# Optimization experiments

Hardware: AMD Instinct MI355X
Metric: run time of the kernel (lower is better)

Reference implementation:

```python
import jax, jax.numpy as jnp
import numpy as np

BN_EPS = 1e-5


def spmm(rows, cols, vals, x):
    # Sparse [V,V] @ x for x: [B, V, F]. COO (rows, cols, vals) with E nnz.
    B, V, F = x.shape
    xt = jnp.transpose(x, (1, 0, 2)).reshape(V, B * F)      # [V, B*F]
    msg = xt[cols] * vals[:, None]                           # [E, B*F]
    y = jax.ops.segment_sum(msg, rows, num_segments=V)       # [V, B*F]
    return jnp.transpose(y.reshape(V, B, F), (1, 0, 2))      # [B, V, F]


def cheb_conv(rows, cols, vals, x, W, b):
    # Chebyshev graph conv: out = sum_k T_k(L) x @ W[k] + b ; W: [K, Fin, Fout]
    K = W.shape[0]
    x0 = x
    out = jnp.einsum('bvi,io->bvo', x0, W[0])
    if K > 1:
        x1 = spmm(rows, cols, vals, x0)
        out = out + jnp.einsum('bvi,io->bvo', x1, W[1])
        for k in range(2, K):
            x2 = 2.0 * spmm(rows, cols, vals, x1) - x0
            out = out + jnp.einsum('bvi,io->bvo', x2, W[k])
            x0, x1 = x1, x2
    return out + b


def bn_relu(x, gamma, beta):
    # BatchNorm1d (training stats) over (batch, nodes) per channel, then ReLU.
    m = jnp.mean(x, axis=(0, 1))
    v = jnp.var(x, axis=(0, 1))
    y = (x - m) * jax.lax.rsqrt(v + BN_EPS) * gamma + beta
    return jax.nn.relu(y)


def setup_inputs() -> dict:
    key = jax.random.key(0)
    ks = jax.random.split(key, 8)
    V, DEG, B, CIN, COUT = 49152, 20, 2, 128, 64
    x = jax.random.normal(ks[0], (B, V, CIN), dtype=jnp.float32)
    # HEALPix-like sparse Laplacian: diagonal + 20 random neighbors per node
    self_idx = jnp.arange(V, dtype=jnp.int32)
    nbr = jax.random.randint(ks[1], (V * DEG,), 0, V, dtype=jnp.int32)
    rows = jnp.concatenate([self_idx, jnp.repeat(self_idx, DEG)])
    cols = jnp.concatenate([self_idx, nbr])
    vals = jax.random.normal(ks[2], (V * (DEG + 1),), dtype=jnp.float32) * 0.1
    def w(k, shape):
        fan_in = shape[0] * shape[1]
        return jax.random.normal(k, shape, dtype=jnp.float32) * np.float32(np.sqrt(2.0 / fan_in))
    return {
        'x': x, 'rows': rows, 'cols': cols, 'vals': vals,
        'W1': w(ks[3], (1, CIN, COUT)), 'b1': jnp.zeros((COUT,), jnp.float32),
        'g1': jnp.ones((COUT,), jnp.float32), 'be1': jnp.zeros((COUT,), jnp.float32),
        'W2': w(ks[4], (3, COUT, COUT)), 'b2': jnp.zeros((COUT,), jnp.float32),
        'g2': jnp.ones((COUT,), jnp.float32), 'be2': jnp.zeros((COUT,), jnp.float32),
        'W3': w(ks[5], (1, COUT, CIN)), 'b3': jnp.zeros((CIN,), jnp.float32),
        'g3': jnp.ones((CIN,), jnp.float32), 'be3': jnp.zeros((CIN,), jnp.float32),
    }


def reference(x, rows, cols, vals, W1, b1, g1, be1, W2, b2, g2, be2, W3, b3, g3, be3):
    h = bn_relu(cheb_conv(rows, cols, vals, x, W1, b1), g1, be1)   # [B,V,64]
    h = bn_relu(cheb_conv(rows, cols, vals, h, W2, b2), g2, be2)   # [B,V,64]
    h = bn_relu(cheb_conv(rows, cols, vals, h, W3, b3), g3, be3)   # [B,V,128]
    return h
```

## Files before the change

### kernel.cpp

```cpp
#include <hip/hip_runtime.h>

#define VN 49152
#define DEG 20
#define NB 2
#define MROWS (NB * VN)

static constexpr float BN_EPS = 1e-5f;

typedef short bf16x8 __attribute__((ext_vector_type(8)));
typedef float floatx4 __attribute__((ext_vector_type(4)));

__device__ __forceinline__ unsigned short f2bf(float f) {
  unsigned int u = __builtin_bit_cast(unsigned int, f);
  u += 0x7FFFu + ((u >> 16) & 1u);
  return (unsigned short)(u >> 16);
}
__device__ __forceinline__ float bf2f(unsigned short h) {
  unsigned int u = ((unsigned int)h) << 16;
  return __builtin_bit_cast(float, u);
}
__device__ __forceinline__ float bflo(unsigned int u) {
  return __builtin_bit_cast(float, u << 16);
}
__device__ __forceinline__ float bfhi(unsigned int u) {
  return __builtin_bit_cast(float, u & 0xFFFF0000u);
}
__device__ __forceinline__ unsigned int packbf(float a, float b) {
  return (unsigned int)f2bf(a) | ((unsigned int)f2bf(b) << 16);
}


#define LDA1 136
__global__ __launch_bounds__(256) void gemm1(const float* __restrict__ X,
    const float* __restrict__ W, const float* __restrict__ bias,
    unsigned short* __restrict__ Y, float* __restrict__ part) {
  __shared__ unsigned short As[128 * LDA1];
  __shared__ unsigned short Bs[64 * LDA1];
  __shared__ float sred[128];
  int t = threadIdx.x;
  int row0 = blockIdx.x * 128;
  if (t < 128) sred[t] = 0.f;
  const float* Xt = X + (size_t)row0 * 128;
  #pragma unroll
  for (int c = 0; c < 16; ++c) {
    int f4i = c * 256 + t;
    int row = f4i >> 5, k = (f4i & 31) * 4;
    float4 v = *(const float4*)(Xt + row * 128 + k);
    unsigned int p0 = packbf(v.x, v.y);
    unsigned int p1 = packbf(v.z, v.w);
    *(uint2*)(&As[row * LDA1 + k]) = make_uint2(p0, p1);
  }
  #pragma unroll
  for (int c = 0; c < 32; ++c) {
    int f = c * 256 + t;
    int k = f >> 6, n = f & 63;
    Bs[n * LDA1 + k] = f2bf(W[f]);
  }
  __syncthreads();
  int l = t & 63, wv = t >> 6;
  int lr = l & 15, q = l >> 4;
  int m0 = wv * 32;
  floatx4 acc[2][4];
  #pragma unroll
  for (int mi = 0; mi < 2; ++mi)
    #pragma unroll
    for (int ni = 0; ni < 4; ++ni) acc[mi][ni] = (floatx4)(0.f);
  #pragma unroll
  for (int ks = 0; ks < 128; ks += 32) {
    bf16x8 af[2], bfr[4];
    #pragma unroll
    for (int mi = 0; mi < 2; ++mi)
      af[mi] = *(const bf16x8*)(&As[(m0 + mi * 16 + lr) * LDA1 + ks + q * 8]);
    #pragma unroll
    for (int ni = 0; ni < 4; ++ni)
      bfr[ni] = *(const bf16x8*)(&Bs[(ni * 16 + lr) * LDA1 + ks + q * 8]);
    #pragma unroll
    for (int mi = 0; mi < 2; ++mi)
      #pragma unroll
      for (int ni = 0; ni < 4; ++ni)
        acc[mi][ni] = __builtin_amdgcn_mfma_f32_16x16x32_bf16(af[mi], bfr[ni], acc[mi][ni], 0, 0, 0);
  }
  int b = (row0 >= VN) ? 1 : 0;
  int vbase = row0 - b * VN + m0;
  #pragma unroll
  for (int ni = 0; ni < 4; ++ni) {
    int col = ni * 16 + lr;
    float bv = bias[col];
    size_t sub = (size_t)(b * 2 + (col >> 5)) * VN;
    float s = 0.f, s2 = 0.f;
    #pragma unroll
    for (int mi = 0; mi < 2; ++mi)
      #pragma unroll
      for (int r = 0; r < 4; ++r) {
        float y = acc[mi][ni][r] + bv;
        s += y; s2 += y * y;
        int v = vbase + mi * 16 + q * 4 + r;
        Y[(sub + v) * 32 + (col & 31)] = f2bf(y);
      }
    atomicAdd(&sred[col], s);
    atomicAdd(&sred[64 + col], s2);
  }
  __syncthreads();
  if (t < 128) part[(size_t)blockIdx.x * 128 + t] = sred[t];
}

#define LDA2 72
__global__ __launch_bounds__(256) void gemm2(const unsigned short* __restrict__ X0,
    const unsigned short* __restrict__ X1, const unsigned short* __restrict__ X2,
    const float* __restrict__ W, const float* __restrict__ bias,
    unsigned short* __restrict__ Y, float* __restrict__ part) {
  __shared__ unsigned short As[128 * LDA2];
  __shared__ unsigned short Bs[64 * LDA2];
  __shared__ float sred[128];
  int t = threadIdx.x;
  int row0 = blockIdx.x * 128;
  int b = (row0 >= VN) ? 1 : 0;
  int b2 = b * 2;
  int vb0 = row0 - b * VN;
  if (t < 128) sred[t] = 0.f;
  int l = t & 63, wv = t >> 6;
  int lr = l & 15, q = l >> 4;
  int m0 = wv * 32;
  floatx4 acc[2][4];
  #pragma unroll
  for (int mi = 0; mi < 2; ++mi)
    #pragma unroll
    for (int ni = 0; ni < 4; ++ni) acc[mi][ni] = (floatx4)(0.f);

  for (int term = 0; term < 3; ++term) {
    const unsigned short* Xp = (term == 0) ? X0 : (term == 1) ? X1 : X2;
    const float* Wt = W + term * 64 * 64;
    #pragma unroll
    for (int c8 = 0; c8 < 8; ++c8) {
      int i = c8 * 256 + t;
      int row = i >> 4, k = (i & 15) * 4;
      const unsigned short* src = Xp + ((size_t)(b2 + (k >> 5)) * VN + vb0 + row) * 32 + (k & 31);
      *(uint2*)(&As[row * LDA2 + k]) = *(const uint2*)src;
    }
    #pragma unroll
    for (int c = 0; c < 16; ++c) {
      int f = c * 256 + t;
      int k = f >> 6, n = f & 63;
      Bs[n * LDA2 + k] = f2bf(Wt[f]);
    }
    __syncthreads();
    #pragma unroll
    for (int ks = 0; ks < 64; ks += 32) {
      bf16x8 af[2], bfr[4];
      #pragma unroll
      for (int mi = 0; mi < 2; ++mi)
        af[mi] = *(const bf16x8*)(&As[(m0 + mi * 16 + lr) * LDA2 + ks + q * 8]);
      #pragma unroll
      for (int ni = 0; ni < 4; ++ni)
        bfr[ni] = *(const bf16x8*)(&Bs[(ni * 16 + lr) * LDA2 + ks + q * 8]);
      #pragma unroll
      for (int mi = 0; mi < 2; ++mi)
        #pragma unroll
        for (int ni = 0; ni < 4; ++ni)
          acc[mi][ni] = __builtin_amdgcn_mfma_f32_16x16x32_bf16(af[mi], bfr[ni], acc[mi][ni], 0, 0, 0);
    }
    __syncthreads();
  }
  int vbase = vb0 + m0;
  #pragma unroll
  for (int ni = 0; ni < 4; ++ni) {
    int col = ni * 16 + lr;
    float bv = bias[col];
    size_t sub = (size_t)(b2 + (col >> 5)) * VN;
    float s = 0.f, s2 = 0.f;
    #pragma unroll
    for (int mi = 0; mi < 2; ++mi)
      #pragma unroll
      for (int r = 0; r < 4; ++r) {
        float y = acc[mi][ni][r] + bv;
        s += y; s2 += y * y;
        int v = vbase + mi * 16 + q * 4 + r;
        Y[(sub + v) * 32 + (col & 31)] = f2bf(y);
      }
    atomicAdd(&sred[col], s);
    atomicAdd(&sred[64 + col], s2);
  }
  __syncthreads();
  if (t < 128) part[(size_t)blockIdx.x * 128 + t] = sred[t];
}

__global__ __launch_bounds__(256) void gemm3(const unsigned short* __restrict__ X,
    const float* __restrict__ W, const float* __restrict__ bias,
    const float* __restrict__ scsh, unsigned short* __restrict__ Y,
    float* __restrict__ part) {
  __shared__ unsigned short As[128 * LDA2];
  __shared__ unsigned short Bs[64 * LDA2];
  __shared__ float sred[128];
  int t = threadIdx.x;
  int row0 = blockIdx.x * 128;
  int n0 = blockIdx.y * 64;
  int b = (row0 >= VN) ? 1 : 0;
  int b2 = b * 2;
  int vb0 = row0 - b * VN;
  if (t < 128) sred[t] = 0.f;
  #pragma unroll
  for (int c8 = 0; c8 < 8; ++c8) {
    int i = c8 * 256 + t;
    int row = i >> 4, k = (i & 15) * 4;
    const unsigned short* src = X + ((size_t)(b2 + (k >> 5)) * VN + vb0 + row) * 32 + (k & 31);
    uint2 rawv = *(const uint2*)src;
    float y0 = fmaf(bflo(rawv.x), scsh[k + 0], scsh[64 + k + 0]);
    float y1 = fmaf(bfhi(rawv.x), scsh[k + 1], scsh[64 + k + 1]);
    float y2 = fmaf(bflo(rawv.y), scsh[k + 2], scsh[64 + k + 2]);
    float y3 = fmaf(bfhi(rawv.y), scsh[k + 3], scsh[64 + k + 3]);
    y0 = y0 > 0.f ? y0 : 0.f; y1 = y1 > 0.f ? y1 : 0.f;
    y2 = y2 > 0.f ? y2 : 0.f; y3 = y3 > 0.f ? y3 : 0.f;
    *(uint2*)(&As[row * LDA2 + k]) = make_uint2(packbf(y0, y1), packbf(y2, y3));
  }
  #pragma unroll
  for (int c = 0; c < 16; ++c) {
    int f = c * 256 + t;
    int k = f >> 6, n = f & 63;
    Bs[n * LDA2 + k] = f2bf(W[k * 128 + n0 + n]);
  }
  __syncthreads();
  int l = t & 63, wv = t >> 6;
  int lr = l & 15, q = l >> 4;
  int m0 = wv * 32;
  floatx4 acc[2][4];
  #pragma unroll
  for (int mi = 0; mi < 2; ++mi)
    #pragma unroll
    for (int ni = 0; ni < 4; ++ni) acc[mi][ni] = (floatx4)(0.f);
  #pragma unroll
  for (int ks = 0; ks < 64; ks += 32) {
    bf16x8 af[2], bfr[4];
    #pragma unroll
    for (int mi = 0; mi < 2; ++mi)
      af[mi] = *(const bf16x8*)(&As[(m0 + mi * 16 + lr) * LDA2 + ks + q * 8]);
    #pragma unroll
    for (int ni = 0; ni < 4; ++ni)
      bfr[ni] = *(const bf16x8*)(&Bs[(ni * 16 + lr) * LDA2 + ks + q * 8]);
    #pragma unroll
    for (int mi = 0; mi < 2; ++mi)
      #pragma unroll
      for (int ni = 0; ni < 4; ++ni)
        acc[mi][ni] = __builtin_amdgcn_mfma_f32_16x16x32_bf16(af[mi], bfr[ni], acc[mi][ni], 0, 0, 0);
  }
  #pragma unroll
  for (int ni = 0; ni < 4; ++ni) {
    int lc = ni * 16 + lr;
    int col = n0 + lc;
    float bv = bias[col];
    float s = 0.f, s2 = 0.f;
    #pragma unroll
    for (int mi = 0; mi < 2; ++mi)
      #pragma unroll
      for (int r = 0; r < 4; ++r) {
        float y = acc[mi][ni][r] + bv;
        s += y; s2 += y * y;
        int row = row0 + m0 + mi * 16 + q * 4 + r;
        Y[(size_t)row * 128 + col] = f2bf(y);
      }
    atomicAdd(&sred[lc], s);
    atomicAdd(&sred[64 + lc], s2);
  }
  __syncthreads();
  if (t < 128)
    part[((size_t)blockIdx.y * 768 + blockIdx.x) * 128 + t] = sred[t];
}

__global__ __launch_bounds__(128) void reduce_scsh64(const float* __restrict__ part,
    const float* __restrict__ gamma, const float* __restrict__ beta,
    float* __restrict__ scsh) {
  int t = threadIdx.x;
  const float* p = part + t;
  float a0 = 0.f, a1 = 0.f, a2 = 0.f, a3 = 0.f;
  for (int b = 0; b < 768; b += 4) {
    a0 += p[(size_t)(b + 0) * 128]; a1 += p[(size_t)(b + 1) * 128];
    a2 += p[(size_t)(b + 2) * 128]; a3 += p[(size_t)(b + 3) * 128];
  }
  __shared__ float sm[128];
  sm[t] = (a0 + a1) + (a2 + a3);
  __syncthreads();
  if (t < 64) {
    float mean = sm[t] * (1.f / MROWS);
    float var = sm[64 + t] * (1.f / MROWS) - mean * mean;
    float sc = gamma[t] * rsqrtf(var + BN_EPS);
    scsh[t] = sc;
    scsh[64 + t] = beta[t] - mean * sc;
  }
}

__global__ __launch_bounds__(256) void reduce_scsh128(const float* __restrict__ part,
    const float* __restrict__ gamma, const float* __restrict__ beta,
    float* __restrict__ scsh) {
  int t = threadIdx.x;
  int col = t & 127, s = t >> 7;
  int gy = col >> 6, lc = col & 63;
  const float* p = part + (size_t)gy * 768 * 128 + s * 64 + lc;
  float a0 = 0.f, a1 = 0.f, a2 = 0.f, a3 = 0.f;
  for (int gx = 0; gx < 768; gx += 4) {
    a0 += p[(size_t)(gx + 0) * 128]; a1 += p[(size_t)(gx + 1) * 128];
    a2 += p[(size_t)(gx + 2) * 128]; a3 += p[(size_t)(gx + 3) * 128];
  }
  __shared__ float sm[256];
  sm[s * 128 + col] = (a0 + a1) + (a2 + a3);
  __syncthreads();
  if (t < 128) {
    float mean = sm[t] * (1.f / MROWS);
    float var = sm[128 + t] * (1.f / MROWS) - mean * mean;
    float sc = gamma[t] * rsqrtf(var + BN_EPS);
    scsh[t] = sc;
    scsh[128 + t] = beta[t] - mean * sc;
  }
}

__global__ __launch_bounds__(256) void bn_h1(const unsigned short* __restrict__ T1,
    const float* __restrict__ scsh, unsigned short* __restrict__ H1) {
  int g = blockIdx.x;
  int combo = (g & 7) >> 1;
  int rg = ((g >> 3) << 1) | (g & 1);
  int t = threadIdx.x;
  int wv = t >> 6, lane = t & 63;
  int v = rg * 64 + wv * 16 + (lane >> 2);
  int ch0 = (lane & 3) * 8;
  int cb = (combo & 1) * 32 + ch0;
  size_t off = (size_t)combo * VN * 32 + (size_t)v * 32 + ch0;
  uint4 d = *(const uint4*)(T1 + off);
  float y[8];
  y[0] = fmaf(bflo(d.x), scsh[cb + 0], scsh[64 + cb + 0]);
  y[1] = fmaf(bfhi(d.x), scsh[cb + 1], scsh[64 + cb + 1]);
  y[2] = fmaf(bflo(d.y), scsh[cb + 2], scsh[64 + cb + 2]);
  y[3] = fmaf(bfhi(d.y), scsh[cb + 3], scsh[64 + cb + 3]);
  y[4] = fmaf(bflo(d.z), scsh[cb + 4], scsh[64 + cb + 4]);
  y[5] = fmaf(bfhi(d.z), scsh[cb + 5], scsh[64 + cb + 5]);
  y[6] = fmaf(bflo(d.w), scsh[cb + 6], scsh[64 + cb + 6]);
  y[7] = fmaf(bfhi(d.w), scsh[cb + 7], scsh[64 + cb + 7]);
  #pragma unroll
  for (int j = 0; j < 8; ++j) y[j] = y[j] > 0.f ? y[j] : 0.f;
  uint4 o;
  o.x = packbf(y[0], y[1]); o.y = packbf(y[2], y[3]);
  o.z = packbf(y[4], y[5]); o.w = packbf(y[6], y[7]);
  *(uint4*)(H1 + off) = o;
}

__global__ __launch_bounds__(256) void spmm1(const unsigned short* __restrict__ H1,
    const int* __restrict__ cols, const float* __restrict__ vals,
    unsigned short* __restrict__ X1out) {
  int g = blockIdx.x;
  int combo = (g & 7) >> 1;
  int rg = ((g >> 3) << 1) | (g & 1);
  int t = threadIdx.x;
  int wv = t >> 6, lane = t & 63;
  int v = rg * 64 + wv * 16 + (lane >> 2);
  int ch0 = (lane & 3) * 8;
  const unsigned short* __restrict__ plane = H1 + (size_t)combo * VN * 32;
  float a[8];
  {
    float w0 = vals[v];
    uint4 d = *(const uint4*)(plane + (size_t)v * 32 + ch0);
    a[0] = w0 * bflo(d.x); a[1] = w0 * bfhi(d.x);
    a[2] = w0 * bflo(d.y); a[3] = w0 * bfhi(d.y);
    a[4] = w0 * bflo(d.z); a[5] = w0 * bfhi(d.z);
    a[6] = w0 * bflo(d.w); a[7] = w0 * bfhi(d.w);
  }
  const int*   __restrict__ cp = cols + VN + v * DEG;
  const float* __restrict__ vp = vals + VN + v * DEG;
  #pragma unroll
  for (int j = 0; j < DEG; ++j) {
    int cj = cp[j];
    float wj = vp[j];
    uint4 d = *(const uint4*)(plane + (size_t)cj * 32 + ch0);
    a[0] = fmaf(bflo(d.x), wj, a[0]); a[1] = fmaf(bfhi(d.x), wj, a[1]);
    a[2] = fmaf(bflo(d.y), wj, a[2]); a[3] = fmaf(bfhi(d.y), wj, a[3]);
    a[4] = fmaf(bflo(d.z), wj, a[4]); a[5] = fmaf(bfhi(d.z), wj, a[5]);
    a[6] = fmaf(bflo(d.w), wj, a[6]); a[7] = fmaf(bfhi(d.w), wj, a[7]);
  }
  uint4 o;
  o.x = packbf(a[0], a[1]); o.y = packbf(a[2], a[3]);
  o.z = packbf(a[4], a[5]); o.w = packbf(a[6], a[7]);
  *(uint4*)(X1out + (size_t)combo * VN * 32 + (size_t)v * 32 + ch0) = o;
}

__global__ __launch_bounds__(256) void spmm2(const unsigned short* __restrict__ X1,
    const unsigned short* __restrict__ H1, const int* __restrict__ cols,
    const float* __restrict__ vals, unsigned short* __restrict__ X2out) {
  int g = blockIdx.x;
  int combo = (g & 7) >> 1;
  int rg = ((g >> 3) << 1) | (g & 1);
  int t = threadIdx.x;
  int wv = t >> 6, lane = t & 63;
  int v = rg * 64 + wv * 16 + (lane >> 2);
  int ch0 = (lane & 3) * 8;
  const size_t pbase = (size_t)combo * VN * 32;
  const size_t myoff = pbase + (size_t)v * 32 + ch0;
  const unsigned short* __restrict__ plane = X1 + pbase;
  float a[8];
  {
    float w0 = vals[v];
    uint4 d = *(const uint4*)(X1 + myoff);
    a[0] = w0 * bflo(d.x); a[1] = w0 * bfhi(d.x);
    a[2] = w0 * bflo(d.y); a[3] = w0 * bfhi(d.y);
    a[4] = w0 * bflo(d.z); a[5] = w0 * bfhi(d.z);
    a[6] = w0 * bflo(d.w); a[7] = w0 * bfhi(d.w);
  }
  const int*   __restrict__ cp = cols + VN + v * DEG;
  const float* __restrict__ vp = vals + VN + v * DEG;
  #pragma unroll
  for (int j = 0; j < DEG; ++j) {
    int cj = cp[j];
    float wj = vp[j];
    uint4 d = *(const uint4*)(plane + (size_t)cj * 32 + ch0);
    a[0] = fmaf(bflo(d.x), wj, a[0]); a[1] = fmaf(bfhi(d.x), wj, a[1]);
    a[2] = fmaf(bflo(d.y), wj, a[2]); a[3] = fmaf(bfhi(d.y), wj, a[3]);
    a[4] = fmaf(bflo(d.z), wj, a[4]); a[5] = fmaf(bfhi(d.z), wj, a[5]);
    a[6] = fmaf(bflo(d.w), wj, a[6]); a[7] = fmaf(bfhi(d.w), wj, a[7]);
  }
  uint4 h = *(const uint4*)(H1 + myoff);
  float hh[8] = {bflo(h.x), bfhi(h.x), bflo(h.y), bfhi(h.y),
                 bflo(h.z), bfhi(h.z), bflo(h.w), bfhi(h.w)};
  uint4 o;
  o.x = packbf(2.f * a[0] - hh[0], 2.f * a[1] - hh[1]);
  o.y = packbf(2.f * a[2] - hh[2], 2.f * a[3] - hh[3]);
  o.z = packbf(2.f * a[4] - hh[4], 2.f * a[5] - hh[5]);
  o.w = packbf(2.f * a[6] - hh[6], 2.f * a[7] - hh[7]);
  *(uint4*)(X2out + myoff) = o;
}

__global__ __launch_bounds__(256) void bn_apply_final(const unsigned short* __restrict__ T,
    float* __restrict__ Y, const float* __restrict__ scsh) {
  size_t i4 = ((size_t)blockIdx.x * 256 + threadIdx.x) * 4;
  int c0 = (int)(i4 & 127);
  ushort4 tv = *(const ushort4*)(T + i4);
  unsigned short sv[4] = {tv.x, tv.y, tv.z, tv.w};
  float ov[4];
  #pragma unroll
  for (int j = 0; j < 4; ++j) {
    int c = c0 + j;
    float y = fmaf(bf2f(sv[j]), scsh[c], scsh[128 + c]);
    ov[j] = y > 0.f ? y : 0.f;
  }
  *(float4*)(Y + i4) = make_float4(ov[0], ov[1], ov[2], ov[3]);
}

extern "C" void kernel_launch(void* const* d_in, const int* in_sizes, int n_in,
                              void* d_out, int out_size, void* d_ws, size_t ws_size,
                              hipStream_t stream) {
  const float* x    = (const float*)d_in[0];
  const int*   cols = (const int*)  d_in[2];
  const float* vals = (const float*)d_in[3];
  const float* W1   = (const float*)d_in[4];
  const float* b1   = (const float*)d_in[5];
  const float* g1   = (const float*)d_in[6];
  const float* be1  = (const float*)d_in[7];
  const float* W2   = (const float*)d_in[8];
  const float* b2   = (const float*)d_in[9];
  const float* g2   = (const float*)d_in[10];
  const float* be2  = (const float*)d_in[11];
  const float* W3   = (const float*)d_in[12];
  const float* b3   = (const float*)d_in[13];
  const float* g3   = (const float*)d_in[14];
  const float* be3  = (const float*)d_in[15];
  float* out = (float*)d_out;

  const size_t PL = (size_t)MROWS * 64;
  unsigned short* P0 = (unsigned short*)d_ws;
  unsigned short* PH = P0 + PL;
  unsigned short* P1 = PH + PL;
  unsigned short* P2 = P1 + PL;
  float* part  = (float*)(P2 + 2 * PL);
  float* scsh1 = part + 1536 * 128;
  float* scsh2 = scsh1 + 128;
  float* scsh3 = scsh2 + 128;

  dim3 blk(256);
  int rowb = MROWS / 128;
  int spmm_blocks = 3072;
  int ap128_blocks = (int)(PL * 2 / 4 / 256);

  gemm1<<<rowb, blk, 0, stream>>>(x, W1, b1, P0, part);
  reduce_scsh64<<<1, 128, 0, stream>>>(part, g1, be1, scsh1);
  bn_h1<<<spmm_blocks, blk, 0, stream>>>(P0, scsh1, PH);

  spmm1<<<spmm_blocks, blk, 0, stream>>>(PH, cols, vals, P1);
  spmm2<<<spmm_blocks, blk, 0, stream>>>(P1, PH, cols, vals, P2);
  gemm2<<<rowb, blk, 0, stream>>>(PH, P1, P2, W2, b2, P0, part);
  reduce_scsh64<<<1, 128, 0, stream>>>(part, g2, be2, scsh2);

  dim3 g3grid(rowb, 2);
  gemm3<<<g3grid, blk, 0, stream>>>(P0, W3, b3, scsh2, P2, part);
  reduce_scsh128<<<1, 256, 0, stream>>>(part, g3, be3, scsh3);
  bn_apply_final<<<ap128_blocks, blk, 0, stream>>>(P2, out, scsh3);
}
```

Measured before the change: 288.9 us.

## Replace BN partial-sum reduce kernels with global atomics and vectorize spmm index loads

Each GEMM block now atomically adds its per-channel sum and sum-of-squares into a small global stats buffer, which is zeroed by a memset. This removes the three single-block reduce kernels and their launches. Consumer kernels recompute the BN scale and shift into shared memory at block start. The spmm kernels also preload the 20 neighbor indices and weights as int4/float4 vectors. The trade-offs are atomic contention on 128 addresses, nondeterministic float summation order, and redundant per-block scale computation.

New measurement: 297.2 us. 1.03x slower.

```diff
diff --git a/kernel.cpp b/kernel.cpp
--- a/kernel.cpp
+++ b/kernel.cpp
@@ -33,7 +33,7 @@
 #define LDA1 136
 __global__ __launch_bounds__(256) void gemm1(const float* __restrict__ X,
     const float* __restrict__ W, const float* __restrict__ bias,
-    unsigned short* __restrict__ Y, float* __restrict__ part) {
+    unsigned short* __restrict__ Y, float* __restrict__ st) {
   __shared__ unsigned short As[128 * LDA1];
   __shared__ unsigned short Bs[64 * LDA1];
   __shared__ float sred[128];
@@ -46,9 +46,7 @@
     int f4i = c * 256 + t;
     int row = f4i >> 5, k = (f4i & 31) * 4;
     float4 v = *(const float4*)(Xt + row * 128 + k);
-    unsigned int p0 = packbf(v.x, v.y);
-    unsigned int p1 = packbf(v.z, v.w);
-    *(uint2*)(&As[row * LDA1 + k]) = make_uint2(p0, p1);
+    *(uint2*)(&As[row * LDA1 + k]) = make_uint2(packbf(v.x, v.y), packbf(v.z, v.w));
   }
   #pragma unroll
   for (int c = 0; c < 32; ++c) {
@@ -101,14 +99,14 @@
     atomicAdd(&sred[64 + col], s2);
   }
   __syncthreads();
-  if (t < 128) part[(size_t)blockIdx.x * 128 + t] = sred[t];
+  if (t < 128) atomicAdd(&st[t], sred[t]);
 }
 
 #define LDA2 72
 __global__ __launch_bounds__(256) void gemm2(const unsigned short* __restrict__ X0,
     const unsigned short* __restrict__ X1, const unsigned short* __restrict__ X2,
     const float* __restrict__ W, const float* __restrict__ bias,
-    unsigned short* __restrict__ Y, float* __restrict__ part) {
+    unsigned short* __restrict__ Y, float* __restrict__ st) {
   __shared__ unsigned short As[128 * LDA2];
   __shared__ unsigned short Bs[64 * LDA2];
   __shared__ float sred[128];
@@ -181,16 +179,18 @@
     atomicAdd(&sred[64 + col], s2);
   }
   __syncthreads();
-  if (t < 128) part[(size_t)blockIdx.x * 128 + t] = sred[t];
+  if (t < 128) atomicAdd(&st[t], sred[t]);
 }
 
 __global__ __launch_bounds__(256) void gemm3(const unsigned short* __restrict__ X,
     const float* __restrict__ W, const float* __restrict__ bias,
-    const float* __restrict__ scsh, unsigned short* __restrict__ Y,
-    float* __restrict__ part) {
+    const float* __restrict__ st2, const float* __restrict__ gamma,
+    const float* __restrict__ beta, unsigned short* __restrict__ Y,
+    float* __restrict__ st3) {
   __shared__ unsigned short As[128 * LDA2];
   __shared__ unsigned short Bs[64 * LDA2];
   __shared__ float sred[128];
+  __shared__ float scS[64], shS[64];
   int t = threadIdx.x;
   int row0 = blockIdx.x * 128;
   int n0 = blockIdx.y * 64;
@@ -198,16 +198,24 @@
   int b2 = b * 2;
   int vb0 = row0 - b * VN;
   if (t < 128) sred[t] = 0.f;
+  if (t < 64) {
+    float mean = st2[t] * (1.f / MROWS);
+    float var = st2[64 + t] * (1.f / MROWS) - mean * mean;
+    float sc = gamma[t] * rsqrtf(var + BN_EPS);
+    scS[t] = sc;
+    shS[t] = beta[t] - mean * sc;
+  }
+  __syncthreads();
   #pragma unroll
   for (int c8 = 0; c8 < 8; ++c8) {
     int i = c8 * 256 + t;
     int row = i >> 4, k = (i & 15) * 4;
     const unsigned short* src = X + ((size_t)(b2 + (k >> 5)) * VN + vb0 + row) * 32 + (k & 31);
     uint2 rawv = *(const uint2*)src;
-    float y0 = fmaf(bflo(rawv.x), scsh[k + 0], scsh[64 + k + 0]);
-    float y1 = fmaf(bfhi(rawv.x), scsh[k + 1], scsh[64 + k + 1]);
-    float y2 = fmaf(bflo(rawv.y), scsh[k + 2], scsh[64 + k + 2]);
-    float y3 = fmaf(bfhi(rawv.y), scsh[k + 3], scsh[64 + k + 3]);
+    float y0 = fmaf(bflo(rawv.x), scS[k + 0], shS[k + 0]);
+    float y1 = fmaf(bfhi(rawv.x), scS[k + 1], shS[k + 1]);
+    float y2 = fmaf(bflo(rawv.y), scS[k + 2], shS[k + 2]);
+    float y3 = fmaf(bfhi(rawv.y), scS[k + 3], shS[k + 3]);
     y0 = y0 > 0.f ? y0 : 0.f; y1 = y1 > 0.f ? y1 : 0.f;
     y2 = y2 > 0.f ? y2 : 0.f; y3 = y3 > 0.f ? y3 : 0.f;
     *(uint2*)(&As[row * LDA2 + k]) = make_uint2(packbf(y0, y1), packbf(y2, y3));
@@ -261,62 +269,25 @@
     atomicAdd(&sred[64 + lc], s2);
   }
   __syncthreads();
-  if (t < 128)
-    part[((size_t)blockIdx.y * 768 + blockIdx.x) * 128 + t] = sred[t];
-}
-
-__global__ __launch_bounds__(128) void reduce_scsh64(const float* __restrict__ part,
-    const float* __restrict__ gamma, const float* __restrict__ beta,
-    float* __restrict__ scsh) {
-  int t = threadIdx.x;
-  const float* p = part + t;
-  float a0 = 0.f, a1 = 0.f, a2 = 0.f, a3 = 0.f;
-  for (int b = 0; b < 768; b += 4) {
-    a0 += p[(size_t)(b + 0) * 128]; a1 += p[(size_t)(b + 1) * 128];
-    a2 += p[(size_t)(b + 2) * 128]; a3 += p[(size_t)(b + 3) * 128];
-  }
-  __shared__ float sm[128];
-  sm[t] = (a0 + a1) + (a2 + a3);
-  __syncthreads();
+  if (t < 128) atomicAdd(&st3[n0 + ((t >> 6) << 7) + (t & 63)], sred[t]);
+}
+
+__global__ __launch_bounds__(256) void bn_h1(const unsigned short* __restrict__ T1,
+    const float* __restrict__ st1, const float* __restrict__ gamma,
+    const float* __restrict__ beta, unsigned short* __restrict__ H1) {
+  __shared__ float scS[64], shS[64];
+  int t = threadIdx.x;
   if (t < 64) {
-    float mean = sm[t] * (1.f / MROWS);
-    float var = sm[64 + t] * (1.f / MROWS) - mean * mean;
+    float mean = st1[t] * (1.f / MROWS);
+    float var = st1[64 + t] * (1.f / MROWS) - mean * mean;
     float sc = gamma[t] * rsqrtf(var + BN_EPS);
-    scsh[t] = sc;
-    scsh[64 + t] = beta[t] - mean * sc;
-  }
-}
-
-__global__ __launch_bounds__(256) void reduce_scsh128(const float* __restrict__ part,
-    const float* __restrict__ gamma, const float* __restrict__ beta,
-    float* __restrict__ scsh) {
-  int t = threadIdx.x;
-  int col = t & 127, s = t >> 7;
-  int gy = col >> 6, lc = col & 63;
-  const float* p = part + (size_t)gy * 768 * 128 + s * 64 + lc;
-  float a0 = 0.f, a1 = 0.f, a2 = 0.f, a3 = 0.f;
-  for (int gx = 0; gx < 768; gx += 4) {
-    a0 += p[(size_t)(gx + 0) * 128]; a1 += p[(size_t)(gx + 1) * 128];
-    a2 += p[(size_t)(gx + 2) * 128]; a3 += p[(size_t)(gx + 3) * 128];
-  }
-  __shared__ float sm[256];
-  sm[s * 128 + col] = (a0 + a1) + (a2 + a3);
-  __syncthreads();
-  if (t < 128) {
-    float mean = sm[t] * (1.f / MROWS);
-    float var = sm[128 + t] * (1.f / MROWS) - mean * mean;
-    float sc = gamma[t] * rsqrtf(var + BN_EPS);
-    scsh[t] = sc;
-    scsh[128 + t] = beta[t] - mean * sc;
-  }
-}
-
-__global__ __launch_bounds__(256) void bn_h1(const unsigned short* __restrict__ T1,
-    const float* __restrict__ scsh, unsigned short* __restrict__ H1) {
+    scS[t] = sc;
+    shS[t] = beta[t] - mean * sc;
+  }
+  __syncthreads();
   int g = blockIdx.x;
   int combo = (g & 7) >> 1;
   int rg = ((g >> 3) << 1) | (g & 1);
-  int t = threadIdx.x;
   int wv = t >> 6, lane = t & 63;
   int v = rg * 64 + wv * 16 + (lane >> 2);
   int ch0 = (lane & 3) * 8;
@@ -324,14 +295,14 @@
   size_t off = (size_t)combo * VN * 32 + (size_t)v * 32 + ch0;
   uint4 d = *(const uint4*)(T1 + off);
   float y[8];
-  y[0] = fmaf(bflo(d.x), scsh[cb + 0], scsh[64 + cb + 0]);
-  y[1] = fmaf(bfhi(d.x), scsh[cb + 1], scsh[64 + cb + 1]);
-  y[2] = fmaf(bflo(d.y), scsh[cb + 2], scsh[64 + cb + 2]);
-  y[3] = fmaf(bfhi(d.y), scsh[cb + 3], scsh[64 + cb + 3]);
-  y[4] = fmaf(bflo(d.z), scsh[cb + 4], scsh[64 + cb + 4]);
-  y[5] = fmaf(bfhi(d.z), scsh[cb + 5], scsh[64 + cb + 5]);
-  y[6] = fmaf(bflo(d.w), scsh[cb + 6], scsh[64 + cb + 6]);
-  y[7] = fmaf(bfhi(d.w), scsh[cb + 7], scsh[64 + cb + 7]);
+  y[0] = fmaf(bflo(d.x), scS[cb + 0], shS[cb + 0]);
+  y[1] = fmaf(bfhi(d.x), scS[cb + 1], shS[cb + 1]);
+  y[2] = fmaf(bflo(d.y), scS[cb + 2], shS[cb + 2]);
+  y[3] = fmaf(bfhi(d.y), scS[cb + 3], shS[cb + 3]);
+  y[4] = fmaf(bflo(d.z), scS[cb + 4], shS[cb + 4]);
+  y[5] = fmaf(bfhi(d.z), scS[cb + 5], shS[cb + 5]);
+  y[6] = fmaf(bflo(d.w), scS[cb + 6], shS[cb + 6]);
+  y[7] = fmaf(bfhi(d.w), scS[cb + 7], shS[cb + 7]);
   #pragma unroll
   for (int j = 0; j < 8; ++j) y[j] = y[j] > 0.f ? y[j] : 0.f;
   uint4 o;
@@ -351,6 +322,12 @@
   int v = rg * 64 + wv * 16 + (lane >> 2);
   int ch0 = (lane & 3) * 8;
   const unsigned short* __restrict__ plane = H1 + (size_t)combo * VN * 32;
+  int4  c4[5];
+  float4 w4[5];
+  const int4*   __restrict__ cp4 = (const int4*)(cols + VN + v * DEG);
+  const float4* __restrict__ vp4 = (const float4*)(vals + VN + v * DEG);
+  #pragma unroll
+  for (int j = 0; j < 5; ++j) { c4[j] = cp4[j]; w4[j] = vp4[j]; }
   float a[8];
   {
     float w0 = vals[v];
@@ -360,17 +337,19 @@
     a[4] = w0 * bflo(d.z); a[5] = w0 * bfhi(d.z);
     a[6] = w0 * bflo(d.w); a[7] = w0 * bfhi(d.w);
   }
-  const int*   __restrict__ cp = cols + VN + v * DEG;
-  const float* __restrict__ vp = vals + VN + v * DEG;
-  #pragma unroll
-  for (int j = 0; j < DEG; ++j) {
-    int cj = cp[j];
-    float wj = vp[j];
-    uint4 d = *(const uint4*)(plane + (size_t)cj * 32 + ch0);
-    a[0] = fmaf(bflo(d.x), wj, a[0]); a[1] = fmaf(bfhi(d.x), wj, a[1]);
-    a[2] = fmaf(bflo(d.y), wj, a[2]); a[3] = fmaf(bfhi(d.y), wj, a[3]);
-    a[4] = fmaf(bflo(d.z), wj, a[4]); a[5] = fmaf(bfhi(d.z), wj, a[5]);
-    a[6] = fmaf(bflo(d.w), wj, a[6]); a[7] = fmaf(bfhi(d.w), wj, a[7]);
+  #pragma unroll
+  for (int j = 0; j < 5; ++j) {
+    const int cj[4] = {c4[j].x, c4[j].y, c4[j].z, c4[j].w};
+    const float wj[4] = {w4[j].x, w4[j].y, w4[j].z, w4[j].w};
+    #pragma unroll
+    for (int e = 0; e < 4; ++e) {
+      uint4 d = *(const uint4*)(plane + (size_t)cj[e] * 32 + ch0);
+      float w = wj[e];
+      a[0] = fmaf(bflo(d.x), w, a[0]); a[1] = fmaf(bfhi(d.x), w, a[1]);
+      a[2] = fmaf(bflo(d.y), w, a[2]); a[3] = fmaf(bfhi(d.y), w, a[3]);
+      a[4] = fmaf(bflo(d.z), w, a[4]); a[5] = fmaf(bfhi(d.z), w, a[5]);
+      a[6] = fmaf(bflo(d.w), w, a[6]); a[7] = fmaf(bfhi(d.w), w, a[7]);
+    }
   }
   uint4 o;
   o.x = packbf(a[0], a[1]); o.y = packbf(a[2], a[3]);
@@ -391,6 +370,12 @@
   const size_t pbase = (size_t)combo * VN * 32;
   const size_t myoff = pbase + (size_t)v * 32 + ch0;
   const unsigned short* __restrict__ plane = X1 + pbase;
+  int4  c4[5];
+  float4 w4[5];
+  const int4*   __restrict__ cp4 = (const int4*)(cols + VN + v * DEG);
+  const float4* __restrict__ vp4 = (const float4*)(vals + VN + v * DEG);
+  #pragma unroll
+  for (int j = 0; j < 5; ++j) { c4[j] = cp4[j]; w4[j] = vp4[j]; }
   float a[8];
   {
     float w0 = vals[v];
@@ -400,32 +385,43 @@
     a[4] = w0 * bflo(d.z); a[5] = w0 * bfhi(d.z);
     a[6] = w0 * bflo(d.w); a[7] = w0 * bfhi(d.w);
   }
-  const int*   __restrict__ cp = cols + VN + v * DEG;
-  const float* __restrict__ vp = vals + VN + v * DEG;
-  #pragma unroll
-  for (int j = 0; j < DEG; ++j) {
-    int cj = cp[j];
-    float wj = vp[j];
-    uint4 d = *(const uint4*)(plane + (size_t)cj * 32 + ch0);
-    a[0] = fmaf(bflo(d.x), wj, a[0]); a[1] = fmaf(bfhi(d.x), wj, a[1]);
-    a[2] = fmaf(bflo(d.y), wj, a[2]); a[3] = fmaf(bfhi(d.y), wj, a[3]);
-    a[4] = fmaf(bflo(d.z), wj, a[4]); a[5] = fmaf(bfhi(d.z), wj, a[5]);
-    a[6] = fmaf(bflo(d.w), wj, a[6]); a[7] = fmaf(bfhi(d.w), wj, a[7]);
+  #pragma unroll
+  for (int j = 0; j < 5; ++j) {
+    const int cj[4] = {c4[j].x, c4[j].y, c4[j].z, c4[j].w};
+    const float wj[4] = {w4[j].x, w4[j].y, w4[j].z, w4[j].w};
+    #pragma unroll
+    for (int e = 0; e < 4; ++e) {
+      uint4 d = *(const uint4*)(plane + (size_t)cj[e] * 32 + ch0);
+      float w = wj[e];
+      a[0] = fmaf(bflo(d.x), w, a[0]); a[1] = fmaf(bfhi(d.x), w, a[1]);
+      a[2] = fmaf(bflo(d.y), w, a[2]); a[3] = fmaf(bfhi(d.y), w, a[3]);
+      a[4] = fmaf(bflo(d.z), w, a[4]); a[5] = fmaf(bfhi(d.z), w, a[5]);
+      a[6] = fmaf(bflo(d.w), w, a[6]); a[7] = fmaf(bfhi(d.w), w, a[7]);
+    }
   }
   uint4 h = *(const uint4*)(H1 + myoff);
-  float hh[8] = {bflo(h.x), bfhi(h.x), bflo(h.y), bfhi(h.y),
-                 bflo(h.z), bfhi(h.z), bflo(h.w), bfhi(h.w)};
   uint4 o;
-  o.x = packbf(2.f * a[0] - hh[0], 2.f * a[1] - hh[1]);
-  o.y = packbf(2.f * a[2] - hh[2], 2.f * a[3] - hh[3]);
-  o.z = packbf(2.f * a[4] - hh[4], 2.f * a[5] - hh[5]);
-  o.w = packbf(2.f * a[6] - hh[6], 2.f * a[7] - hh[7]);
+  o.x = packbf(2.f * a[0] - bflo(h.x), 2.f * a[1] - bfhi(h.x));
+  o.y = packbf(2.f * a[2] - bflo(h.y), 2.f * a[3] - bfhi(h.y));
+  o.z = packbf(2.f * a[4] - bflo(h.z), 2.f * a[5] - bfhi(h.z));
+  o.w = packbf(2.f * a[6] - bflo(h.w), 2.f * a[7] - bfhi(h.w));
   *(uint4*)(X2out + myoff) = o;
 }
 
-__global__ __launch_bounds__(256) void bn_apply_final(const unsigned short* __restrict__ T,
-    float* __restrict__ Y, const float* __restrict__ scsh) {
-  size_t i4 = ((size_t)blockIdx.x * 256 + threadIdx.x) * 4;
+__global__ __launch_bounds__(256) void bn_final(const unsigned short* __restrict__ T,
+    float* __restrict__ Y, const float* __restrict__ st3,
+    const float* __restrict__ gamma, const float* __restrict__ beta) {
+  __shared__ float scS[128], shS[128];
+  int t = threadIdx.x;
+  if (t < 128) {
+    float mean = st3[t] * (1.f / MROWS);
+    float var = st3[128 + t] * (1.f / MROWS) - mean * mean;
+    float sc = gamma[t] * rsqrtf(var + BN_EPS);
+    scS[t] = sc;
+    shS[t] = beta[t] - mean * sc;
+  }
+  __syncthreads();
+  size_t i4 = ((size_t)blockIdx.x * 256 + t) * 4;
   int c0 = (int)(i4 & 127);
   ushort4 tv = *(const ushort4*)(T + i4);
   unsigned short sv[4] = {tv.x, tv.y, tv.z, tv.w};
@@ -433,7 +429,7 @@
   #pragma unroll
   for (int j = 0; j < 4; ++j) {
     int c = c0 + j;
-    float y = fmaf(bf2f(sv[j]), scsh[c], scsh[128 + c]);
+    float y = fmaf(bf2f(sv[j]), scS[c], shS[c]);
     ov[j] = y > 0.f ? y : 0.f;
   }
   *(float4*)(Y + i4) = make_float4(ov[0], ov[1], ov[2], ov[3]);
@@ -464,27 +460,25 @@
   unsigned short* PH = P0 + PL;
   unsigned short* P1 = PH + PL;
   unsigned short* P2 = P1 + PL;
-  float* part  = (float*)(P2 + 2 * PL);
-  float* scsh1 = part + 1536 * 128;
-  float* scsh2 = scsh1 + 128;
-  float* scsh3 = scsh2 + 128;
+  float* st1 = (float*)(P2 + 2 * PL);
+  float* st2 = st1 + 128;
+  float* st3 = st2 + 128;
+
+  hipMemsetAsync(st1, 0, 512 * sizeof(float), stream);
 
   dim3 blk(256);
   int rowb = MROWS / 128;
   int spmm_blocks = 3072;
   int ap128_blocks = (int)(PL * 2 / 4 / 256);
 
-  gemm1<<<rowb, blk, 0, stream>>>(x, W1, b1, P0, part);
-  reduce_scsh64<<<1, 128, 0, stream>>>(part, g1, be1, scsh1);
-  bn_h1<<<spmm_blocks, blk, 0, stream>>>(P0, scsh1, PH);
+  gemm1<<<rowb, blk, 0, stream>>>(x, W1, b1, P0, st1);
+  bn_h1<<<spmm_blocks, blk, 0, stream>>>(P0, st1, g1, be1, PH);
 
   spmm1<<<spmm_blocks, blk, 0, stream>>>(PH, cols, vals, P1);
   spmm2<<<spmm_blocks, blk, 0, stream>>>(P1, PH, cols, vals, P2);
-  gemm2<<<rowb, blk, 0, stream>>>(PH, P1, P2, W2, b2, P0, part);
-  reduce_scsh64<<<1, 128, 0, stream>>>(part, g2, be2, scsh2);
+  gemm2<<<rowb, blk, 0, stream>>>(PH, P1, P2, W2, b2, P0, st2);
 
   dim3 g3grid(rowb, 2);
-  gemm3<<<g3grid, blk, 0, stream>>>(P0, W3, b3, scsh2, P2, part);
-  reduce_scsh128<<<1, 256, 0, stream>>>(part, g3, be3, scsh3);
-  bn_apply_final<<<ap128_blocks, blk, 0, stream>>>(P2, out, scsh3);
-}
+  gemm3<<<g3grid, blk, 0, stream>>>(P0, W3, b3, st2, g2, be2, P2, st3);
+  bn_final<<<ap128_blocks, blk, 0, stream>>>(P2, out, st3, g3, be3);
+}
```
